# Optimization experiments

Measured on AMD Instinct MI355X. Metric: run time of the kernel, lower is better.

The kernel has to match this reference:

```python
import jax, jax.numpy as jnp
import numpy as np

DIM = 768
HEADS = 12
HIDDEN = 4 * DIM
B, N = 8, 1024
EPS = 1e-5


def setup_inputs() -> dict:
    key = jax.random.key(0)
    ks = jax.random.split(key, 8)
    s = 0.02
    return {
        "x": jax.random.normal(ks[0], (B, N, DIM), dtype=jnp.float32),
        "ln1_g": jnp.ones((DIM,), jnp.float32),
        "ln1_b": jnp.zeros((DIM,), jnp.float32),
        "qkv_w": jax.random.normal(ks[1], (3 * DIM, DIM), jnp.float32) * s,
        "proj_w": jax.random.normal(ks[2], (DIM, DIM), jnp.float32) * s,
        "proj_b": jnp.zeros((DIM,), jnp.float32),
        "ln2_g": jnp.ones((DIM,), jnp.float32),
        "ln2_b": jnp.zeros((DIM,), jnp.float32),
        "fc1_w": jax.random.normal(ks[3], (HIDDEN, DIM), jnp.float32) * s,
        "fc1_b": jnp.zeros((HIDDEN,), jnp.float32),
        "fc2_w": jax.random.normal(ks[4], (DIM, HIDDEN), jnp.float32) * s,
        "fc2_b": jnp.zeros((DIM,), jnp.float32),
    }


def _layernorm(x, g, b):
    mu = jnp.mean(x, axis=-1, keepdims=True)
    var = jnp.mean(jnp.square(x - mu), axis=-1, keepdims=True)
    return (x - mu) * jax.lax.rsqrt(var + EPS) * g + b


def reference(x, ln1_g, ln1_b, qkv_w, proj_w, proj_b, ln2_g, ln2_b, fc1_w, fc1_b, fc2_w, fc2_b):
    Bn, Nn, C = x.shape
    H = HEADS
    D = C // H
    scale = D ** -0.5

    # --- attention branch ---
    h = _layernorm(x, ln1_g, ln1_b)
    qkv = h @ qkv_w.T                      # [B,N,3C] (qkv_bias=False)
    qkv = qkv.reshape(Bn, Nn, 3, H, D)
    q = qkv[:, :, 0].transpose(0, 2, 1, 3)  # [B,H,N,D]
    k = qkv[:, :, 1].transpose(0, 2, 1, 3)
    v = qkv[:, :, 2].transpose(0, 2, 1, 3)
    attn = jnp.einsum('bhnd,bhmd->bhnm', q, k) * scale  # [B,H,N,N]
    attn = jax.nn.softmax(attn, axis=-1)
    ctx = jnp.einsum('bhnm,bhmd->bhnd', attn, v)         # [B,H,N,D]
    ctx = ctx.transpose(0, 2, 1, 3).reshape(Bn, Nn, C)
    x = x + ctx @ proj_w.T + proj_b

    # --- MLP branch ---
    h = _layernorm(x, ln2_g, ln2_b)
    h = jax.nn.gelu(h @ fc1_w.T + fc1_b, approximate=False)
    return x + h @ fc2_w.T + fc2_b
```

## Files before the change

### kernel.cpp

```cpp
#include <hip/hip_runtime.h>
#include <cstdint>

typedef __attribute__((ext_vector_type(8))) short short8;
typedef __attribute__((ext_vector_type(4))) float f32x4;
typedef unsigned short u16t;

__device__ __forceinline__ u16t f2bf(float f) {
  uint32_t u = __float_as_uint(f);
  u += 0x7fffu + ((u >> 16) & 1u);
  return (u16t)(u >> 16);
}

__device__ __forceinline__ void gload_lds16(const void* g, void* l) {
  __builtin_amdgcn_global_load_lds(
      (const __attribute__((address_space(1))) void*)g,
      (__attribute__((address_space(3))) void*)l, 16, 0, 0);
}

__global__ __launch_bounds__(256) void cvt_bf16_kernel(const float* __restrict__ in,
                                                       u16t* __restrict__ out, int n8) {
  int i = blockIdx.x * 256 + threadIdx.x;
  if (i >= n8) return;
  const float4* p = (const float4*)in + (size_t)i * 2;
  float4 a = p[0], b = p[1];
  union { short8 v; u16t e[8]; } r;
  r.e[0] = f2bf(a.x); r.e[1] = f2bf(a.y); r.e[2] = f2bf(a.z); r.e[3] = f2bf(a.w);
  r.e[4] = f2bf(b.x); r.e[5] = f2bf(b.y); r.e[6] = f2bf(b.z); r.e[7] = f2bf(b.w);
  *((short8*)out + i) = r.v;
}

__global__ __launch_bounds__(256) void ln_kernel(const float* __restrict__ x,
                                                 const float* __restrict__ g,
                                                 const float* __restrict__ b,
                                                 u16t* __restrict__ out) {
  int row = blockIdx.x, tid = threadIdx.x;
  int wave = tid >> 6, lane = tid & 63;
  const float* xr = x + (size_t)row * 768;
  float v0 = xr[tid], v1 = xr[tid + 256], v2 = xr[tid + 512];
  float s = v0 + v1 + v2;
  float q = v0 * v0 + v1 * v1 + v2 * v2;
#pragma unroll
  for (int m = 32; m >= 1; m >>= 1) {
    s += __shfl_xor(s, m, 64);
    q += __shfl_xor(q, m, 64);
  }
  __shared__ float red[8];
  if (lane == 0) { red[wave] = s; red[4 + wave] = q; }
  __syncthreads();
  s = red[0] + red[1] + red[2] + red[3];
  q = red[4] + red[5] + red[6] + red[7];
  float mu = s * (1.0f / 768.0f);
  float var = q * (1.0f / 768.0f) - mu * mu;
  float rs = rsqrtf(var + 1e-5f);
  u16t* orow = out + (size_t)row * 768;
  orow[tid]       = f2bf((v0 - mu) * rs * g[tid]       + b[tid]);
  orow[tid + 256] = f2bf((v1 - mu) * rs * g[tid + 256] + b[tid + 256]);
  orow[tid + 512] = f2bf((v2 - mu) * rs * g[tid + 512] + b[tid + 512]);
}

template <int EPI>
__global__ __launch_bounds__(256, 2) void gemm_bt(const u16t* __restrict__ A,
                                                  const u16t* __restrict__ W,
                                                  void* __restrict__ Cout,
                                                  const float* __restrict__ bias,
                                                  const float* __restrict__ res,
                                                  int M, int N, int K) {
  __shared__ __align__(16) u16t As[128 * 64];
  __shared__ __align__(16) u16t Bs[128 * 64];
  int tid = threadIdx.x;
  int wave = tid >> 6, lane = tid & 63;
  int wr = wave >> 1, wc = wave & 1;
  int bm = blockIdx.y * 128;
  int bn = blockIdx.x * 128;
  f32x4 acc[4][4] = {};

  int lr = lane >> 3;
  int lc = lane & 7;
  int srcslot = lc ^ lr;
  const u16t* Abase = A + (size_t)(bm + lr) * K + srcslot * 8;
  const u16t* Wbase = W + (size_t)(bn + lr) * K + srcslot * 8;

  for (int kt = 0; kt < K; kt += 64) {
    __syncthreads();
#pragma unroll
    for (int i = 0; i < 4; i++) {
      int chunk = wave * 4 + i;
      gload_lds16(Abase + (size_t)(chunk * 8) * K + kt, (void*)(As + chunk * 512));
      gload_lds16(Wbase + (size_t)(chunk * 8) * K + kt, (void*)(Bs + chunk * 512));
    }
    __syncthreads();

    short8 af[4][2], bfr[4][2];
#pragma unroll
    for (int m = 0; m < 4; m++) {
      int row = wr * 64 + m * 16 + (lane & 15);
#pragma unroll
      for (int s = 0; s < 2; s++) {
        int slot = s * 4 + (lane >> 4);
        af[m][s] = *(const short8*)(As + row * 64 + ((slot ^ (row & 7)) * 8));
      }
    }
#pragma unroll
    for (int n = 0; n < 4; n++) {
      int row = wc * 64 + n * 16 + (lane & 15);
#pragma unroll
      for (int s = 0; s < 2; s++) {
        int slot = s * 4 + (lane >> 4);
        bfr[n][s] = *(const short8*)(Bs + row * 64 + ((slot ^ (row & 7)) * 8));
      }
    }
#pragma unroll
    for (int m = 0; m < 4; m++)
#pragma unroll
      for (int n = 0; n < 4; n++) {
        acc[m][n] = __builtin_amdgcn_mfma_f32_16x16x32_bf16(af[m][0], bfr[n][0], acc[m][n], 0, 0, 0);
        acc[m][n] = __builtin_amdgcn_mfma_f32_16x16x32_bf16(af[m][1], bfr[n][1], acc[m][n], 0, 0, 0);
      }
  }

#pragma unroll
  for (int m = 0; m < 4; m++) {
#pragma unroll
    for (int n = 0; n < 4; n++) {
      int r0 = bm + wr * 64 + m * 16 + (lane >> 4) * 4;
      int c = bn + wc * 64 + n * 16 + (lane & 15);
#pragma unroll
      for (int i = 0; i < 4; i++) {
        int r = r0 + i;
        float v = acc[m][n][i];
        if constexpr (EPI == 0) {
          ((u16t*)Cout)[(size_t)r * N + c] = f2bf(v);
        } else if constexpr (EPI == 1) {
          ((float*)Cout)[(size_t)r * N + c] = v + bias[c] + res[(size_t)r * N + c];
        } else {
          v += bias[c];
          float gl = 0.5f * v * (1.0f + erff(v * 0.70710678118f));
          ((u16t*)Cout)[(size_t)r * N + c] = f2bf(gl);
        }
      }
    }
  }
}

__global__ __launch_bounds__(256, 2) void attn_kernel(const u16t* __restrict__ qkv,
                                                      u16t* __restrict__ ctx) {
  __shared__ __align__(16) u16t Ks[64 * 64];
  __shared__ __align__(16) u16t Vt[64 * 72];
  __shared__ __align__(16) u16t Ps[4][16 * 72];
  int tid = threadIdx.x;
  int wave = tid >> 6, lane = tid & 63;
  int b = blockIdx.x / 12, h = blockIdx.x % 12;
  int qt = blockIdx.y * 64;
  const u16t* base = qkv + (size_t)b * 1024 * 2304 + h * 64;

  int qrow = qt + wave * 16 + (lane & 15);
  const u16t* qp = base + (size_t)qrow * 2304 + (lane >> 4) * 8;
  short8 aq0 = *(const short8*)qp;
  short8 aq1 = *(const short8*)(qp + 32);

  const u16t* kbase = base + 768;
  const u16t* vbase = base + 1536;
  int lr = lane >> 3, lc = lane & 7;
  const u16t* kst = kbase + (size_t)lr * 2304 + ((lc ^ lr) * 8);
  const u16t* vst = vbase + (size_t)lane * 2304 + wave * 16;

  float m_i[4] = {-1e30f, -1e30f, -1e30f, -1e30f};
  float l_i[4] = {0.f, 0.f, 0.f, 0.f};
  f32x4 o[4] = {};
  const float scale = 0.125f;
  u16t* Pw = Ps[wave];

  for (int kt = 0; kt < 1024; kt += 64) {
    __syncthreads();
#pragma unroll
    for (int i = 0; i < 2; i++) {
      int chunk = wave * 2 + i;
      gload_lds16(kst + (size_t)(kt + chunk * 8) * 2304, (void*)(Ks + chunk * 512));
    }
    {
      const u16t* vp = vst + (size_t)kt * 2304;
      union { uint4 u; u16t e[8]; } v0u, v1u;
      v0u.u = *(const uint4*)vp;
      v1u.u = *(const uint4*)(vp + 8);
#pragma unroll
      for (int j = 0; j < 8; j++) Vt[(wave * 16 + j) * 72 + lane] = v0u.e[j];
#pragma unroll
      for (int j = 0; j < 8; j++) Vt[(wave * 16 + 8 + j) * 72 + lane] = v1u.e[j];
    }
    __syncthreads();

    f32x4 s[4] = {};
#pragma unroll
    for (int n = 0; n < 4; n++) {
      int row = n * 16 + (lane & 15);
      int s0 = (lane >> 4);
      short8 bk0 = *(const short8*)(Ks + row * 64 + ((s0 ^ (row & 7)) * 8));
      short8 bk1 = *(const short8*)(Ks + row * 64 + (((s0 + 4) ^ (row & 7)) * 8));
      s[n] = __builtin_amdgcn_mfma_f32_16x16x32_bf16(aq0, bk0, s[n], 0, 0, 0);
      s[n] = __builtin_amdgcn_mfma_f32_16x16x32_bf16(aq1, bk1, s[n], 0, 0, 0);
    }

    float alpha[4];
#pragma unroll
    for (int i = 0; i < 4; i++) {
      float mt = fmaxf(fmaxf(s[0][i], s[1][i]), fmaxf(s[2][i], s[3][i]));
      mt = fmaxf(mt, __shfl_xor(mt, 1, 64));
      mt = fmaxf(mt, __shfl_xor(mt, 2, 64));
      mt = fmaxf(mt, __shfl_xor(mt, 4, 64));
      mt = fmaxf(mt, __shfl_xor(mt, 8, 64));
      float mnew = fmaxf(m_i[i], mt * scale);
      alpha[i] = __expf(m_i[i] - mnew);
      m_i[i] = mnew;
    }
    float rsum[4] = {0.f, 0.f, 0.f, 0.f};
#pragma unroll
    for (int n = 0; n < 4; n++)
#pragma unroll
      for (int i = 0; i < 4; i++) {
        float p = __expf(s[n][i] * scale - m_i[i]);
        s[n][i] = p;
        rsum[i] += p;
      }
#pragma unroll
    for (int i = 0; i < 4; i++) {
      rsum[i] += __shfl_xor(rsum[i], 1, 64);
      rsum[i] += __shfl_xor(rsum[i], 2, 64);
      rsum[i] += __shfl_xor(rsum[i], 4, 64);
      rsum[i] += __shfl_xor(rsum[i], 8, 64);
      l_i[i] = l_i[i] * alpha[i] + rsum[i];
    }
#pragma unroll
    for (int n = 0; n < 4; n++)
#pragma unroll
      for (int i = 0; i < 4; i++)
        Pw[((lane >> 4) * 4 + i) * 72 + n * 16 + (lane & 15)] = f2bf(s[n][i]);
#pragma unroll
    for (int nd = 0; nd < 4; nd++)
#pragma unroll
      for (int i = 0; i < 4; i++) o[nd][i] *= alpha[i];
#pragma unroll
    for (int st = 0; st < 2; st++) {
      short8 ap = *(const short8*)(Pw + (lane & 15) * 72 + st * 32 + (lane >> 4) * 8);
#pragma unroll
      for (int nd = 0; nd < 4; nd++) {
        short8 bv = *(const short8*)(Vt + (nd * 16 + (lane & 15)) * 72 + st * 32 + (lane >> 4) * 8);
        o[nd] = __builtin_amdgcn_mfma_f32_16x16x32_bf16(ap, bv, o[nd], 0, 0, 0);
      }
    }
  }

#pragma unroll
  for (int i = 0; i < 4; i++) l_i[i] = 1.0f / l_i[i];
  int q0 = qt + wave * 16 + (lane >> 4) * 4;
#pragma unroll
  for (int i = 0; i < 4; i++) {
    u16t* crow = ctx + (size_t)(b * 1024 + q0 + i) * 768 + h * 64;
#pragma unroll
    for (int nd = 0; nd < 4; nd++)
      crow[nd * 16 + (lane & 15)] = f2bf(o[nd][i] * l_i[i]);
  }
}

extern "C" void kernel_launch(void* const* d_in, const int* in_sizes, int n_in,
                              void* d_out, int out_size, void* d_ws, size_t ws_size,
                              hipStream_t stream) {
  const float* x      = (const float*)d_in[0];
  const float* ln1_g  = (const float*)d_in[1];
  const float* ln1_b  = (const float*)d_in[2];
  const float* qkv_w  = (const float*)d_in[3];
  const float* proj_w = (const float*)d_in[4];
  const float* proj_b = (const float*)d_in[5];
  const float* ln2_g  = (const float*)d_in[6];
  const float* ln2_b  = (const float*)d_in[7];
  const float* fc1_w  = (const float*)d_in[8];
  const float* fc1_b  = (const float*)d_in[9];
  const float* fc2_w  = (const float*)d_in[10];
  const float* fc2_b  = (const float*)d_in[11];

  char* ws = (char*)d_ws;
  u16t* h1   = (u16t*)(ws + 0);
  u16t* qkvb = (u16t*)(ws + 12582912);
  u16t* ctx  = (u16t*)(ws + 50331648);
  float* x2  = (float*)(ws + 62914560);
  u16t* hid  = (u16t*)(ws + 88080384);
  u16t* wq   = (u16t*)(ws + 138412032);
  u16t* wp   = (u16t*)(ws + 141950976);
  u16t* w1   = (u16t*)(ws + 143130624);
  u16t* w2   = (u16t*)(ws + 147849216);
  float* out = (float*)d_out;

  cvt_bf16_kernel<<<864, 256, 0, stream>>>(qkv_w, wq, 221184);
  cvt_bf16_kernel<<<288, 256, 0, stream>>>(proj_w, wp, 73728);
  cvt_bf16_kernel<<<1152, 256, 0, stream>>>(fc1_w, w1, 294912);
  cvt_bf16_kernel<<<1152, 256, 0, stream>>>(fc2_w, w2, 294912);

  ln_kernel<<<8192, 256, 0, stream>>>(x, ln1_g, ln1_b, h1);
  gemm_bt<0><<<dim3(18, 64), 256, 0, stream>>>(h1, wq, qkvb, nullptr, nullptr, 8192, 2304, 768);
  attn_kernel<<<dim3(96, 16), 256, 0, stream>>>(qkvb, ctx);
  gemm_bt<1><<<dim3(6, 64), 256, 0, stream>>>(ctx, wp, x2, proj_b, x, 8192, 768, 768);
  ln_kernel<<<8192, 256, 0, stream>>>(x2, ln2_g, ln2_b, h1);
  gemm_bt<2><<<dim3(24, 64), 256, 0, stream>>>(h1, w1, hid, fc1_b, nullptr, 8192, 3072, 768);
  gemm_bt<1><<<dim3(6, 64), 256, 0, stream>>>(hid, w2, out, fc2_b, x2, 8192, 768, 3072);
}
```

Measured before the change: 308.1 us.

## Double-buffer K/V tiles in attention, use 64-row tiles for N=768 GEMMs

The attention kernel now double-buffers the K and V tiles in shared memory, prefetching the next tile into registers and LDS while the current tile is computed, with one barrier per iteration. The GEMM gains a BM template parameter so the two output-width-768 GEMMs use 64-row tiles, doubling their grid from 384 to 768 blocks to fill the CUs better. s_setprio hints wrap the MFMA sections. Costs are more LDS in attention, which may affect occupancy, and less reuse per block in the smaller GEMM tiles.

```diff
diff --git a/kernel.cpp b/kernel.cpp
--- a/kernel.cpp
+++ b/kernel.cpp
@@ -58,21 +58,22 @@
   orow[tid + 512] = f2bf((v2 - mu) * rs * g[tid + 512] + b[tid + 512]);
 }
 
-template <int EPI>
+template <int EPI, int BM>
 __global__ __launch_bounds__(256, 2) void gemm_bt(const u16t* __restrict__ A,
                                                   const u16t* __restrict__ W,
                                                   void* __restrict__ Cout,
                                                   const float* __restrict__ bias,
                                                   const float* __restrict__ res,
                                                   int M, int N, int K) {
-  __shared__ __align__(16) u16t As[128 * 64];
+  __shared__ __align__(16) u16t As[BM * 64];
   __shared__ __align__(16) u16t Bs[128 * 64];
+  constexpr int MF = BM / 32;
   int tid = threadIdx.x;
   int wave = tid >> 6, lane = tid & 63;
   int wr = wave >> 1, wc = wave & 1;
-  int bm = blockIdx.y * 128;
+  int bm = blockIdx.y * BM;
   int bn = blockIdx.x * 128;
-  f32x4 acc[4][4] = {};
+  f32x4 acc[MF][4] = {};
 
   int lr = lane >> 3;
   int lc = lane & 7;
@@ -83,17 +84,21 @@
   for (int kt = 0; kt < K; kt += 64) {
     __syncthreads();
 #pragma unroll
+    for (int i = 0; i < BM / 32; i++) {
+      int chunk = wave * (BM / 32) + i;
+      gload_lds16(Abase + (size_t)(chunk * 8) * K + kt, (void*)(As + chunk * 512));
+    }
+#pragma unroll
     for (int i = 0; i < 4; i++) {
       int chunk = wave * 4 + i;
-      gload_lds16(Abase + (size_t)(chunk * 8) * K + kt, (void*)(As + chunk * 512));
       gload_lds16(Wbase + (size_t)(chunk * 8) * K + kt, (void*)(Bs + chunk * 512));
     }
     __syncthreads();
 
-    short8 af[4][2], bfr[4][2];
-#pragma unroll
-    for (int m = 0; m < 4; m++) {
-      int row = wr * 64 + m * 16 + (lane & 15);
+    short8 af[MF][2], bfr[4][2];
+#pragma unroll
+    for (int m = 0; m < MF; m++) {
+      int row = wr * (BM / 2) + m * 16 + (lane & 15);
 #pragma unroll
       for (int s = 0; s < 2; s++) {
         int slot = s * 4 + (lane >> 4);
@@ -109,20 +114,22 @@
         bfr[n][s] = *(const short8*)(Bs + row * 64 + ((slot ^ (row & 7)) * 8));
       }
     }
-#pragma unroll
-    for (int m = 0; m < 4; m++)
+    __builtin_amdgcn_s_setprio(1);
+#pragma unroll
+    for (int m = 0; m < MF; m++)
 #pragma unroll
       for (int n = 0; n < 4; n++) {
         acc[m][n] = __builtin_amdgcn_mfma_f32_16x16x32_bf16(af[m][0], bfr[n][0], acc[m][n], 0, 0, 0);
         acc[m][n] = __builtin_amdgcn_mfma_f32_16x16x32_bf16(af[m][1], bfr[n][1], acc[m][n], 0, 0, 0);
       }
-  }
-
-#pragma unroll
-  for (int m = 0; m < 4; m++) {
+    __builtin_amdgcn_s_setprio(0);
+  }
+
+#pragma unroll
+  for (int m = 0; m < MF; m++) {
 #pragma unroll
     for (int n = 0; n < 4; n++) {
-      int r0 = bm + wr * 64 + m * 16 + (lane >> 4) * 4;
+      int r0 = bm + wr * (BM / 2) + m * 16 + (lane >> 4) * 4;
       int c = bn + wc * 64 + n * 16 + (lane & 15);
 #pragma unroll
       for (int i = 0; i < 4; i++) {
@@ -144,8 +151,8 @@
 
 __global__ __launch_bounds__(256, 2) void attn_kernel(const u16t* __restrict__ qkv,
                                                       u16t* __restrict__ ctx) {
-  __shared__ __align__(16) u16t Ks[64 * 64];
-  __shared__ __align__(16) u16t Vt[64 * 72];
+  __shared__ __align__(16) u16t Ks[2][64 * 64];
+  __shared__ __align__(16) u16t Vt[2][64 * 72];
   __shared__ __align__(16) u16t Ps[4][16 * 72];
   int tid = threadIdx.x;
   int wave = tid >> 6, lane = tid & 63;
@@ -170,35 +177,52 @@
   const float scale = 0.125f;
   u16t* Pw = Ps[wave];
 
-  for (int kt = 0; kt < 1024; kt += 64) {
-    __syncthreads();
+  union { uint4 u; u16t e[8]; } v0u, v1u;
+
+  auto loadV = [&](int kt) {
+    const u16t* vp = vst + (size_t)kt * 2304;
+    v0u.u = *(const uint4*)vp;
+    v1u.u = *(const uint4*)(vp + 8);
+  };
+  auto stageK = [&](int kt, int buf) {
 #pragma unroll
     for (int i = 0; i < 2; i++) {
       int chunk = wave * 2 + i;
-      gload_lds16(kst + (size_t)(kt + chunk * 8) * 2304, (void*)(Ks + chunk * 512));
-    }
-    {
-      const u16t* vp = vst + (size_t)kt * 2304;
-      union { uint4 u; u16t e[8]; } v0u, v1u;
-      v0u.u = *(const uint4*)vp;
-      v1u.u = *(const uint4*)(vp + 8);
-#pragma unroll
-      for (int j = 0; j < 8; j++) Vt[(wave * 16 + j) * 72 + lane] = v0u.e[j];
-#pragma unroll
-      for (int j = 0; j < 8; j++) Vt[(wave * 16 + 8 + j) * 72 + lane] = v1u.e[j];
-    }
-    __syncthreads();
-
+      gload_lds16(kst + (size_t)(kt + chunk * 8) * 2304, (void*)(Ks[buf] + chunk * 512));
+    }
+  };
+  auto writeV = [&](int buf) {
+#pragma unroll
+    for (int j = 0; j < 8; j++) Vt[buf][(wave * 16 + j) * 72 + lane] = v0u.e[j];
+#pragma unroll
+    for (int j = 0; j < 8; j++) Vt[buf][(wave * 16 + 8 + j) * 72 + lane] = v1u.e[j];
+  };
+
+  loadV(0);
+  stageK(0, 0);
+  writeV(0);
+  __syncthreads();
+
+  for (int t = 0; t < 16; ++t) {
+    int buf = t & 1;
+    if (t < 15) {
+      loadV((t + 1) * 64);
+      stageK((t + 1) * 64, buf ^ 1);
+    }
+
+    const u16t* Kb = Ks[buf];
     f32x4 s[4] = {};
+    __builtin_amdgcn_s_setprio(1);
 #pragma unroll
     for (int n = 0; n < 4; n++) {
       int row = n * 16 + (lane & 15);
       int s0 = (lane >> 4);
-      short8 bk0 = *(const short8*)(Ks + row * 64 + ((s0 ^ (row & 7)) * 8));
-      short8 bk1 = *(const short8*)(Ks + row * 64 + (((s0 + 4) ^ (row & 7)) * 8));
+      short8 bk0 = *(const short8*)(Kb + row * 64 + ((s0 ^ (row & 7)) * 8));
+      short8 bk1 = *(const short8*)(Kb + row * 64 + (((s0 + 4) ^ (row & 7)) * 8));
       s[n] = __builtin_amdgcn_mfma_f32_16x16x32_bf16(aq0, bk0, s[n], 0, 0, 0);
       s[n] = __builtin_amdgcn_mfma_f32_16x16x32_bf16(aq1, bk1, s[n], 0, 0, 0);
     }
+    __builtin_amdgcn_s_setprio(0);
 
     float alpha[4];
 #pragma unroll
@@ -238,15 +262,21 @@
     for (int nd = 0; nd < 4; nd++)
 #pragma unroll
       for (int i = 0; i < 4; i++) o[nd][i] *= alpha[i];
+    const u16t* Vb = Vt[buf];
+    __builtin_amdgcn_s_setprio(1);
 #pragma unroll
     for (int st = 0; st < 2; st++) {
       short8 ap = *(const short8*)(Pw + (lane & 15) * 72 + st * 32 + (lane >> 4) * 8);
 #pragma unroll
       for (int nd = 0; nd < 4; nd++) {
-        short8 bv = *(const short8*)(Vt + (nd * 16 + (lane & 15)) * 72 + st * 32 + (lane >> 4) * 8);
+        short8 bv = *(const short8*)(Vb + (nd * 16 + (lane & 15)) * 72 + st * 32 + (lane >> 4) * 8);
         o[nd] = __builtin_amdgcn_mfma_f32_16x16x32_bf16(ap, bv, o[nd], 0, 0, 0);
       }
     }
+    __builtin_amdgcn_s_setprio(0);
+
+    if (t < 15) writeV(buf ^ 1);
+    __syncthreads();
   }
 
 #pragma unroll
@@ -295,10 +325,10 @@
   cvt_bf16_kernel<<<1152, 256, 0, stream>>>(fc2_w, w2, 294912);
 
   ln_kernel<<<8192, 256, 0, stream>>>(x, ln1_g, ln1_b, h1);
-  gemm_bt<0><<<dim3(18, 64), 256, 0, stream>>>(h1, wq, qkvb, nullptr, nullptr, 8192, 2304, 768);
+  gemm_bt<0, 128><<<dim3(18, 64), 256, 0, stream>>>(h1, wq, qkvb, nullptr, nullptr, 8192, 2304, 768);
   attn_kernel<<<dim3(96, 16), 256, 0, stream>>>(qkvb, ctx);
-  gemm_bt<1><<<dim3(6, 64), 256, 0, stream>>>(ctx, wp, x2, proj_b, x, 8192, 768, 768);
+  gemm_bt<1, 64><<<dim3(6, 128), 256, 0, stream>>>(ctx, wp, x2, proj_b, x, 8192, 768, 768);
   ln_kernel<<<8192, 256, 0, stream>>>(x2, ln2_g, ln2_b, h1);
-  gemm_bt<2><<<dim3(24, 64), 256, 0, stream>>>(h1, w1, hid, fc1_b, nullptr, 8192, 3072, 768);
-  gemm_bt<1><<<dim3(6, 64), 256, 0, stream>>>(hid, w2, out, fc2_b, x2, 8192, 768, 3072);
-}
+  gemm_bt<2, 128><<<dim3(24, 64), 256, 0, stream>>>(h1, w1, hid, fc1_b, nullptr, 8192, 3072, 768);
+  gemm_bt<1, 64><<<dim3(6, 128), 256, 0, stream>>>(hid, w2, out, fc2_b, x2, 8192, 768, 3072);
+}
```

After: 305.9 us. Within noise of the previous version (-0.7%).
